# Performance work log

Measured on AMD Instinct MI355X. Metric: run time of the kernel, lower is better.

The kernel has to match this reference:

```python
import jax, jax.numpy as jnp
import numpy as np

DROPOUT_RATE = 0.5
CONF_THRESH = 0.85
IGNORE_VALUE = 2
EPS = 1e-07


def setup_inputs() -> dict:
    key = jax.random.key(0)
    k1, k2 = jax.random.split(key)
    B, H, W = 16, 1024, 1024
    pred = jax.random.uniform(k1, (B, H, W), dtype=jnp.float32)
    mask = jax.random.randint(k2, (B, H, W), 0, 3, dtype=jnp.int32)
    return {"pred": pred, "mask": mask}


def _training_need_score(pred, gt, confidence):
    # Higher = needs more training: CW=4, UW=3, UC=2, CC=1 (+/- confidence bonus)
    is_correct = (pred > 0.5) == (gt == 1.0)
    is_conf = confidence > CONF_THRESH
    score = jnp.where(is_conf & is_correct, 1.0,
            jnp.where(~is_conf & is_correct, 2.0,
            jnp.where(~is_conf & ~is_correct, 3.0, 4.0))).astype(pred.dtype)
    bonus = (confidence - 0.5) * 0.5
    return jnp.where(is_correct, score - bonus, score + bonus)


def _dynamic_masks(pred, mask):
    # Vectorized equivalent of the per-batch nonzero/argsort/scatter loop:
    # rank annotated pixels per batch by descending need-score; top n_train -> train.
    B, H, W = mask.shape
    annotated = (mask != IGNORE_VALUE).reshape(B, H * W)
    gt = mask.astype(pred.dtype)
    confidence = jnp.maximum(pred, 1.0 - pred)
    scores = _training_need_score(pred, gt, confidence).reshape(B, H * W)
    neg_inf = jnp.asarray(-jnp.inf, scores.dtype)
    masked_scores = jnp.where(annotated, scores, neg_inf)
    order = jnp.argsort(-masked_scores, axis=1)          # descending score order
    rank = jnp.argsort(order, axis=1)                    # rank of each pixel in that order
    n_points = annotated.sum(axis=1)
    n_train = (n_points.astype(jnp.float32) * (1.0 - DROPOUT_RATE)).astype(jnp.int32)
    train = annotated & (rank < n_train[:, None])
    holdout = annotated & ~train
    return train.reshape(B, H, W), holdout.reshape(B, H, W)


def reference(pred, mask):
    if pred.ndim == 4 and pred.shape[1] == 1:
        pred = pred[:, 0]
    train_mask, holdout_mask = _dynamic_masks(pred, mask)
    gt = mask.astype(pred.dtype)
    p = jnp.clip(pred, EPS, 1.0 - EPS)
    bce = -(gt * jnp.log(p) + (1.0 - gt) * jnp.log(1.0 - p))
    tm = train_mask.astype(pred.dtype)
    loss = (bce * tm).sum() / (tm.sum() + EPS)
    return loss, train_mask, holdout_mask
```

## Files before the change

### kernel.cpp

```cpp
#include <hip/hip_runtime.h>
#include <stdint.h>

#define NBATCH 16
#define HW_ (1 << 20)
#define TPB 256

#define NBPB_H 64
#define EPB_H (HW_ / NBPB_H)
#define ITER_H (EPB_H / (TPB * 4))

#define NBINS 8192
#define FBASE 0x3F400

#define NBPB_F 256
#define FCHUNK (HW_ / NBPB_F)

#define CAND_CAP 32768
#define LCAP 512
#define TIE_CAP 4096
#define CSTR 64

typedef float f4v __attribute__((ext_vector_type(4)));

struct BParams {
    unsigned int k;
    unsigned int bin1f;
    unsigned int r;
    unsigned int mode;
};

__device__ __forceinline__ unsigned int score_bits(float p, int m) {
    bool correct = (p > 0.5f) == (m == 1);
    float conf = fmaxf(p, 1.0f - p);
    float base = correct ? ((conf > 0.85f) ? 1.0f : 2.0f)
                         : ((conf > 0.85f) ? 4.0f : 3.0f);
    float bonus = (conf - 0.5f) * 0.5f;
    float s = correct ? (base - bonus) : (base + bonus);
    return __float_as_uint(s);
}

__global__ void k_hist1(const float4* __restrict__ pred4, const int4* __restrict__ mask4,
                        unsigned int* __restrict__ hist1) {
    __shared__ unsigned int lh[NBINS];
    int b = blockIdx.x / NBPB_H;
    int blk = blockIdx.x % NBPB_H;
    for (int i = threadIdx.x; i < NBINS; i += TPB) lh[i] = 0;
    __syncthreads();
    int l4base = blk * (EPB_H / 4);
    for (int j = 0; j < ITER_H; j++) {
        int i4l = l4base + j * TPB + threadIdx.x;
        size_t g4 = (size_t)b * (HW_ / 4) + i4l;
        float4 p = pred4[g4];
        int4 m = mask4[g4];
        float pa[4] = {p.x, p.y, p.z, p.w};
        int ma[4] = {m.x, m.y, m.z, m.w};
#pragma unroll
        for (int l = 0; l < 4; l++) {
            if (ma[l] != 2) {
                unsigned int sb = score_bits(pa[l], ma[l]);
                int fb = (int)(sb >> 12) - FBASE;
                fb = min(max(fb, 0), NBINS - 1);
                atomicAdd(&lh[fb], 1u);
            }
        }
    }
    __syncthreads();
    for (int i = threadIdx.x; i < NBINS; i += TPB) {
        unsigned int v = lh[i];
        if (v) atomicAdd(&hist1[b * NBINS + i], v);
    }
}

__global__ void k_find1(const unsigned int* __restrict__ hist1, BParams* prm) {
    int b = blockIdx.x;
    int t = threadIdx.x;
    __shared__ unsigned int cs_[257];
    const unsigned int* h = hist1 + (size_t)b * NBINS;
    {
        const uint4* h4 = (const uint4*)(h + t * 32);
        unsigned int s = 0;
#pragma unroll
        for (int j = 0; j < 8; j++) { uint4 v = h4[j]; s += v.x + v.y + v.z + v.w; }
        cs_[t] = s;
        if (t == 0) cs_[256] = 0;
    }
    __syncthreads();
    for (int off = 1; off < 256; off <<= 1) {
        unsigned int a = (t + off < 256) ? cs_[t + off] : 0u;
        __syncthreads();
        cs_[t] += a;
        __syncthreads();
    }
    unsigned int n = cs_[0];
    unsigned int k = (unsigned int)(int)((float)n * 0.5f);
    if (k == 0) {
        if (t == 0) {
            BParams P;
            P.k = 0; P.bin1f = 0xFFFFFFFFu; P.r = 0; P.mode = 0;
            prm[b] = P;
        }
        return;
    }
    if (cs_[t] >= k && cs_[t + 1] < k) {
        unsigned int cum = cs_[t + 1];
        for (int j = 31; j >= 0; j--) {
            unsigned int hb = h[t * 32 + j];
            if (cum + hb >= k) {
                BParams P;
                P.k = k;
                P.bin1f = (unsigned int)(FBASE + t * 32 + j);
                P.r = k - cum;
                P.mode = 1;
                prm[b] = P;
                break;
            }
            cum += hb;
        }
    }
}

__global__ void k_main(const float4* __restrict__ pred4, const int4* __restrict__ mask4,
                       const BParams* __restrict__ prm, float* __restrict__ out,
                       float* __restrict__ partials, unsigned int* __restrict__ cand_cnt,
                       unsigned int* __restrict__ cand_idx, unsigned int* __restrict__ cand_sb,
                       float* __restrict__ cand_bce) {
    int b = blockIdx.x / NBPB_F;
    int blk = blockIdx.x % NBPB_F;
    BParams P = prm[b];
    unsigned int target = P.bin1f;
    __shared__ unsigned int lcode[FCHUNK / 4];
    __shared__ float red[TPB];
    __shared__ unsigned int l_idx[LCAP];
    __shared__ unsigned int l_sb[LCAP];
    __shared__ float l_bce[LCAP];
    __shared__ unsigned int lcnt;
    __shared__ unsigned int gbase;
    if (threadIdx.x == 0) lcnt = 0;
    __syncthreads();
    float acc = 0.0f;
    int ibase = blk * FCHUNK;
    for (int j = 0; j < FCHUNK / (TPB * 4); j++) {
        int v = j * TPB + threadIdx.x;
        size_t g4 = (size_t)b * (HW_ / 4) + (ibase / 4) + v;
        float4 p = pred4[g4];
        int4 m = mask4[g4];
        float pa[4] = {p.x, p.y, p.z, p.w};
        int ma[4] = {m.x, m.y, m.z, m.w};
        unsigned int cw = 0;
#pragma unroll
        for (int l = 0; l < 4; l++) {
            bool ann = (ma[l] != 2);
            unsigned int sb = score_bits(pa[l], ma[l]);
            unsigned int fine = sb >> 12;
            bool tr = ann && (fine > target);
            bool amb = ann && (fine == target);
            unsigned int code = (tr ? 1u : 0u) | ((ann && !tr) ? 2u : 0u);
            cw |= code << (8 * l);
            float bce = 0.0f;
            if (tr || amb) {
                float pc = fminf(fmaxf(pa[l], 1e-7f), 1.0f - 1e-7f);
                bce = (ma[l] == 1) ? -__logf(pc) : -__logf(1.0f - pc);
            }
            if (tr) acc += bce;
            if (amb) {
                unsigned int p0 = atomicAdd(&lcnt, 1u);
                if (p0 < LCAP) {
                    l_idx[p0] = (unsigned int)(ibase + v * 4 + l);
                    l_sb[p0] = sb;
                    l_bce[p0] = bce;
                } else {
                    unsigned int gp = atomicAdd(&cand_cnt[b * CSTR], 1u);
                    if (gp < CAND_CAP) {
                        size_t o = (size_t)b * CAND_CAP + gp;
                        cand_idx[o] = (unsigned int)(ibase + v * 4 + l);
                        cand_sb[o] = sb;
                        cand_bce[o] = bce;
                    }
                }
            }
        }
        lcode[v] = cw;
    }
    __syncthreads();
    unsigned int n = min(lcnt, (unsigned int)LCAP);
    if (threadIdx.x == 0 && n > 0)
        gbase = atomicAdd(&cand_cnt[b * CSTR], n);
    __syncthreads();
    for (unsigned int i = threadIdx.x; i < n; i += TPB) {
        unsigned int pos = gbase + i;
        if (pos < CAND_CAP) {
            size_t o = (size_t)b * CAND_CAP + pos;
            cand_idx[o] = l_idx[i];
            cand_sb[o] = l_sb[i];
            cand_bce[o] = l_bce[i];
        }
    }
    float* trout = out + 1;
    float* hoout = out + 1 + (size_t)NBATCH * HW_;
    size_t Gbase = (size_t)b * HW_ + (size_t)ibase;
    for (int v = threadIdx.x; v < FCHUNK / 4 - 1; v += TPB) {
        unsigned int w0 = lcode[v];
        unsigned int w1 = lcode[v + 1];
        unsigned int c0 = (w0 >> 24) & 0xFFu;
        unsigned int c1 = w1 & 0xFFu;
        unsigned int c2 = (w1 >> 8) & 0xFFu;
        unsigned int c3 = (w1 >> 16) & 0xFFu;
        int e = 3 + 4 * v;
        f4v tv = { (float)(c0 & 1u), (float)(c1 & 1u), (float)(c2 & 1u), (float)(c3 & 1u) };
        f4v hv = { (float)((c0 >> 1) & 1u), (float)((c1 >> 1) & 1u),
                   (float)((c2 >> 1) & 1u), (float)((c3 >> 1) & 1u) };
        __builtin_nontemporal_store(tv, (f4v*)(trout + Gbase + e));
        __builtin_nontemporal_store(hv, (f4v*)(hoout + Gbase + e));
    }
    if (threadIdx.x < 3) {
        unsigned int c = (lcode[0] >> (8 * threadIdx.x)) & 0xFFu;
        trout[Gbase + threadIdx.x] = (float)(c & 1u);
        hoout[Gbase + threadIdx.x] = (float)((c >> 1) & 1u);
    }
    if (threadIdx.x == 3) {
        unsigned int c = (lcode[FCHUNK / 4 - 1] >> 24) & 0xFFu;
        trout[Gbase + FCHUNK - 1] = (float)(c & 1u);
        hoout[Gbase + FCHUNK - 1] = (float)((c >> 1) & 1u);
    }
    red[threadIdx.x] = acc;
    __syncthreads();
    for (int off = TPB / 2; off > 0; off >>= 1) {
        if (threadIdx.x < off) red[threadIdx.x] += red[threadIdx.x + off];
        __syncthreads();
    }
    if (threadIdx.x == 0) partials[blockIdx.x] = red[0];
}

__global__ void k_fixuploss(const unsigned int* __restrict__ cand_cnt,
                            const unsigned int* __restrict__ cand_idx,
                            const unsigned int* __restrict__ cand_sb,
                            const float* __restrict__ cand_bce,
                            const BParams* __restrict__ prm, float* __restrict__ out,
                            float* __restrict__ tie_partials,
                            const float* __restrict__ partials,
                            unsigned int* __restrict__ doneC) {
    int b = blockIdx.x;
    int t = threadIdx.x;
    __shared__ unsigned int h[4096];
    __shared__ unsigned int cs_[257];
    __shared__ unsigned int tie_idx[TIE_CAP];
    __shared__ unsigned int misc[8];
    __shared__ float red[TPB];
    __shared__ unsigned int lastFlag;
    BParams P = prm[b];
    if (P.mode != 0) {
        unsigned int C = cand_cnt[b * CSTR];
        if (C > CAND_CAP) C = CAND_CAP;
        const unsigned int* ci = cand_idx + (size_t)b * CAND_CAP;
        const unsigned int* cs = cand_sb + (size_t)b * CAND_CAP;
        const float* cb = cand_bce + (size_t)b * CAND_CAP;
        for (int i = t; i < 4096; i += TPB) h[i] = 0;
        if (t < 8) misc[t] = (t == 4) ? 0xFFFFFFFFu : 0u;
        __syncthreads();
        for (unsigned int i = t; i < C; i += TPB)
            atomicAdd(&h[cs[i] & 0xFFFu], 1u);
        __syncthreads();
        {
            unsigned int gs = 0;
#pragma unroll
            for (int j = 0; j < 16; j++) gs += h[t * 16 + j];
            cs_[t] = gs;
            if (t == 0) cs_[256] = 0;
        }
        __syncthreads();
        for (int off = 1; off < 256; off <<= 1) {
            unsigned int a = (t + off < 256) ? cs_[t + off] : 0u;
            __syncthreads();
            cs_[t] += a;
            __syncthreads();
        }
        if (cs_[t] >= P.r && cs_[t + 1] < P.r) {
            unsigned int cum = cs_[t + 1];
            for (int j = 15; j >= 0; j--) {
                unsigned int hb = h[t * 16 + j];
                if (cum + hb >= P.r) {
                    unsigned int T = P.r - cum;
                    misc[0] = (unsigned int)(t * 16 + j);
                    misc[1] = T;
                    misc[2] = (T == hb) ? 1u : 0u;
                    break;
                }
                cum += hb;
            }
        }
        __syncthreads();
        unsigned int vstar = misc[0], T = misc[1];
        bool allTies = (misc[2] != 0);
        unsigned int idxcut;
        if (allTies) {
            idxcut = 0xFFFFFFFFu;
        } else {
            for (unsigned int i = t; i < C; i += TPB) {
                if ((cs[i] & 0xFFFu) == vstar) {
                    unsigned int p = atomicAdd(&misc[3], 1u);
                    if (p < TIE_CAP) tie_idx[p] = ci[i];
                }
            }
            __syncthreads();
            unsigned int E2 = misc[3];
            if (E2 > TIE_CAP) E2 = TIE_CAP;
            for (unsigned int i = t; i < E2; i += TPB) {
                unsigned int vi = tie_idx[i];
                unsigned int cnt = 0;
                for (unsigned int j = 0; j < E2; j++) cnt += (tie_idx[j] < vi) ? 1u : 0u;
                if (cnt == T - 1) misc[4] = vi;
            }
            __syncthreads();
            idxcut = misc[4];
        }
        float acc = 0.0f;
        float* trout = out + 1;
        float* hoout = out + 1 + (size_t)NBATCH * HW_;
        size_t base = (size_t)b * HW_;
        for (unsigned int i = t; i < C; i += TPB) {
            unsigned int low = cs[i] & 0xFFFu;
            bool tr = (low > vstar) || (low == vstar && ci[i] <= idxcut);
            if (tr) {
                trout[base + ci[i]] = 1.0f;
                hoout[base + ci[i]] = 0.0f;
                acc += cb[i];
            }
        }
        red[t] = acc;
        __syncthreads();
        for (int off = TPB / 2; off > 0; off >>= 1) {
            if (t < off) red[t] += red[t + off];
            __syncthreads();
        }
        if (t == 0) tie_partials[b] = red[0];
    } else {
        if (t == 0) tie_partials[b] = 0.0f;
    }
    if (t == 0) {
        __threadfence();
        lastFlag = (atomicAdd(doneC, 1u) == NBATCH - 1) ? 1u : 0u;
    }
    __syncthreads();
    if (!lastFlag) return;
    {
        __shared__ double dred[TPB];
        double s = 0.0;
        for (int i = t; i < NBATCH * NBPB_F; i += TPB) s += (double)partials[i];
        if (t < NBATCH) s += (double)tie_partials[t];
        dred[t] = s;
        __syncthreads();
        for (int off = TPB / 2; off > 0; off >>= 1) {
            if (t < off) dred[t] += dred[t + off];
            __syncthreads();
        }
        if (t == 0) {
            unsigned long long den = 0;
            for (int b2 = 0; b2 < NBATCH; b2++) den += prm[b2].k;
            float denf = (float)den + 1e-7f;
            out[0] = (float)dred[0] / denf;
        }
    }
}

extern "C" void kernel_launch(void* const* d_in, const int* in_sizes, int n_in,
                              void* d_out, int out_size, void* d_ws, size_t ws_size,
                              hipStream_t stream) {
    const float4* pred4 = (const float4*)d_in[0];
    const int4* mask4 = (const int4*)d_in[1];
    float* out = (float*)d_out;

    unsigned int* hist1 = (unsigned int*)d_ws;
    unsigned int* cand_cnt = hist1 + NBATCH * NBINS;
    unsigned int* doneC = cand_cnt + NBATCH * CSTR;
    BParams* prm = (BParams*)(doneC + 64);
    float* partials = (float*)(prm + NBATCH);
    float* tie_partials = partials + NBATCH * NBPB_F;
    unsigned int* cand_idx = (unsigned int*)(tie_partials + NBATCH);
    unsigned int* cand_sb = cand_idx + NBATCH * CAND_CAP;
    float* cand_bce = (float*)(cand_sb + NBATCH * CAND_CAP);

    size_t zero_bytes = (size_t)(NBATCH * NBINS + NBATCH * CSTR + 64) * 4;
    hipMemsetAsync(d_ws, 0, zero_bytes, stream);

    k_hist1<<<dim3(NBATCH * NBPB_H), dim3(TPB), 0, stream>>>(pred4, mask4, hist1);
    k_find1<<<dim3(NBATCH), dim3(TPB), 0, stream>>>(hist1, prm);
    k_main<<<dim3(NBATCH * NBPB_F), dim3(TPB), 0, stream>>>(pred4, mask4, prm, out, partials,
                                                            cand_cnt, cand_idx, cand_sb, cand_bce);
    k_fixuploss<<<dim3(NBATCH), dim3(TPB), 0, stream>>>(cand_cnt, cand_idx, cand_sb, cand_bce,
                                                        prm, out, tie_partials, partials, doneC);
}
```

Before: 290.1 us.

## Fuse histogram and threshold-find kernels via last-block completion counter

Merges the per-batch histogram kernel and the threshold-search kernel into one launch. Each block also adds a 64-bin coarse histogram, and the last block per batch (found with an atomic done counter and a threadfence) scans the coarse bins, then the 128 fine bins of the selected coarse bin, to write the batch parameters. This removes one kernel launch and the separate 8192-bin scan, at the cost of extra coarse atomics, serialized tail work in the last block, and more workspace to zero.

Result: slower. 313.4 us (+8.0%).

```diff
diff --git a/kernel.cpp b/kernel.cpp
--- a/kernel.cpp
+++ b/kernel.cpp
@@ -11,6 +11,7 @@
 
 #define NBINS 8192
 #define FBASE 0x3F400
+#define NCOARSE 64
 
 #define NBPB_F 256
 #define FCHUNK (HW_ / NBPB_F)
@@ -39,16 +40,22 @@
     return __float_as_uint(s);
 }
 
-__global__ void k_hist1(const float4* __restrict__ pred4, const int4* __restrict__ mask4,
-                        unsigned int* __restrict__ hist1) {
+__global__ void k_histfind(const float4* __restrict__ pred4, const int4* __restrict__ mask4,
+                           unsigned int* __restrict__ hist1, unsigned int* __restrict__ coarse,
+                           unsigned int* __restrict__ doneA, BParams* __restrict__ prm) {
     __shared__ unsigned int lh[NBINS];
+    __shared__ unsigned int sc[NCOARSE + 1];
+    __shared__ unsigned int hs[129];
+    __shared__ unsigned int miscF[2];
+    __shared__ unsigned int lastFlag;
     int b = blockIdx.x / NBPB_H;
     int blk = blockIdx.x % NBPB_H;
-    for (int i = threadIdx.x; i < NBINS; i += TPB) lh[i] = 0;
+    int t = threadIdx.x;
+    for (int i = t; i < NBINS; i += TPB) lh[i] = 0;
     __syncthreads();
     int l4base = blk * (EPB_H / 4);
     for (int j = 0; j < ITER_H; j++) {
-        int i4l = l4base + j * TPB + threadIdx.x;
+        int i4l = l4base + j * TPB + t;
         size_t g4 = (size_t)b * (HW_ / 4) + i4l;
         float4 p = pred4[g4];
         int4 m = mask4[g4];
@@ -65,57 +72,69 @@
         }
     }
     __syncthreads();
-    for (int i = threadIdx.x; i < NBINS; i += TPB) {
+    for (int i = t; i < NBINS; i += TPB) {
         unsigned int v = lh[i];
         if (v) atomicAdd(&hist1[b * NBINS + i], v);
     }
-}
-
-__global__ void k_find1(const unsigned int* __restrict__ hist1, BParams* prm) {
-    int b = blockIdx.x;
-    int t = threadIdx.x;
-    __shared__ unsigned int cs_[257];
-    const unsigned int* h = hist1 + (size_t)b * NBINS;
-    {
-        const uint4* h4 = (const uint4*)(h + t * 32);
+    if (t < NCOARSE) {
         unsigned int s = 0;
 #pragma unroll
-        for (int j = 0; j < 8; j++) { uint4 v = h4[j]; s += v.x + v.y + v.z + v.w; }
-        cs_[t] = s;
-        if (t == 0) cs_[256] = 0;
-    }
-    __syncthreads();
-    for (int off = 1; off < 256; off <<= 1) {
-        unsigned int a = (t + off < 256) ? cs_[t + off] : 0u;
-        __syncthreads();
-        cs_[t] += a;
-        __syncthreads();
-    }
-    unsigned int n = cs_[0];
+        for (int jj = 0; jj < 128; jj++) s += lh[t * 128 + ((jj + t) & 127)];
+        if (s) atomicAdd(&coarse[b * CSTR + t], s);
+    }
+    __syncthreads();
+    if (t == 0) {
+        __threadfence();
+        lastFlag = (atomicAdd(&doneA[b * CSTR], 1u) == NBPB_H - 1) ? 1u : 0u;
+    }
+    __syncthreads();
+    if (!lastFlag) return;
+    if (t == 0) __threadfence();
+    __syncthreads();
+
+    if (t < NCOARSE) sc[t] = coarse[b * CSTR + t];
+    if (t == 0) sc[NCOARSE] = 0;
+    __syncthreads();
+    for (int off = 1; off < NCOARSE; off <<= 1) {
+        unsigned int a = 0;
+        if (t < NCOARSE) a = (t + off < NCOARSE) ? sc[t + off] : 0u;
+        __syncthreads();
+        if (t < NCOARSE) sc[t] += a;
+        __syncthreads();
+    }
+    unsigned int n = sc[0];
     unsigned int k = (unsigned int)(int)((float)n * 0.5f);
     if (k == 0) {
         if (t == 0) {
-            BParams P;
-            P.k = 0; P.bin1f = 0xFFFFFFFFu; P.r = 0; P.mode = 0;
+            BParams P; P.k = 0; P.bin1f = 0xFFFFFFFFu; P.r = 0; P.mode = 0;
             prm[b] = P;
         }
         return;
     }
-    if (cs_[t] >= k && cs_[t + 1] < k) {
-        unsigned int cum = cs_[t + 1];
-        for (int j = 31; j >= 0; j--) {
-            unsigned int hb = h[t * 32 + j];
-            if (cum + hb >= k) {
-                BParams P;
-                P.k = k;
-                P.bin1f = (unsigned int)(FBASE + t * 32 + j);
-                P.r = k - cum;
-                P.mode = 1;
-                prm[b] = P;
-                break;
-            }
-            cum += hb;
-        }
+    if (t < NCOARSE && sc[t] >= k && sc[t + 1] < k) {
+        miscF[0] = (unsigned int)t;
+        miscF[1] = sc[t + 1];
+    }
+    __syncthreads();
+    unsigned int cstar = miscF[0];
+    unsigned int rk = k - miscF[1];
+    if (t < 128) hs[t] = hist1[(size_t)b * NBINS + cstar * 128 + t];
+    if (t == 0) hs[128] = 0;
+    __syncthreads();
+    for (int off = 1; off < 128; off <<= 1) {
+        unsigned int a = 0;
+        if (t < 128) a = (t + off < 128) ? hs[t + off] : 0u;
+        __syncthreads();
+        if (t < 128) hs[t] += a;
+        __syncthreads();
+    }
+    if (t < 128 && hs[t] >= rk && hs[t + 1] < rk) {
+        BParams P;
+        P.k = k;
+        P.bin1f = (unsigned int)(FBASE + cstar * 128 + t);
+        P.r = rk - hs[t + 1];
+        P.mode = 1;
+        prm[b] = P;
     }
 }
 
@@ -370,7 +389,9 @@
     float* out = (float*)d_out;
 
     unsigned int* hist1 = (unsigned int*)d_ws;
-    unsigned int* cand_cnt = hist1 + NBATCH * NBINS;
+    unsigned int* coarse = hist1 + NBATCH * NBINS;
+    unsigned int* doneA = coarse + NBATCH * CSTR;
+    unsigned int* cand_cnt = doneA + NBATCH * CSTR;
     unsigned int* doneC = cand_cnt + NBATCH * CSTR;
     BParams* prm = (BParams*)(doneC + 64);
     float* partials = (float*)(prm + NBATCH);
@@ -379,11 +400,11 @@
     unsigned int* cand_sb = cand_idx + NBATCH * CAND_CAP;
     float* cand_bce = (float*)(cand_sb + NBATCH * CAND_CAP);
 
-    size_t zero_bytes = (size_t)(NBATCH * NBINS + NBATCH * CSTR + 64) * 4;
+    size_t zero_bytes = (size_t)(NBATCH * NBINS + 3 * NBATCH * CSTR + 64) * 4;
     hipMemsetAsync(d_ws, 0, zero_bytes, stream);
 
-    k_hist1<<<dim3(NBATCH * NBPB_H), dim3(TPB), 0, stream>>>(pred4, mask4, hist1);
-    k_find1<<<dim3(NBATCH), dim3(TPB), 0, stream>>>(hist1, prm);
+    k_histfind<<<dim3(NBATCH * NBPB_H), dim3(TPB), 0, stream>>>(pred4, mask4, hist1,
+                                                                coarse, doneA, prm);
     k_main<<<dim3(NBATCH * NBPB_F), dim3(TPB), 0, stream>>>(pred4, mask4, prm, out, partials,
                                                             cand_cnt, cand_idx, cand_sb, cand_bce);
     k_fixuploss<<<dim3(NBATCH), dim3(TPB), 0, stream>>>(cand_cnt, cand_idx, cand_sb, cand_bce,
```
